# Kernel optimization log

Measured on AMD Instinct MI355X. Metric: run time of the kernel, lower is better.

## Reference

```python
import jax, jax.numpy as jnp
import numpy as np

B, S, H, I, L, NH = 1, 256, 384, 1536, 2, 8

def _gelu(x):
    return jax.nn.gelu(x, approximate=False)  # torch nn.GELU default = exact erf

def _ln(x, g, b, eps=1e-5):
    m = x.mean(-1, keepdims=True)
    v = jnp.var(x, axis=-1, keepdims=True)
    return (x - m) / jnp.sqrt(v + eps) * g + b

def _mha(x, Wqkv, bqkv, Wo, bo):
    b_, s_, h_ = x.shape
    d = h_ // NH
    qkv = x @ Wqkv.T + bqkv  # [B,S,3H]
    q, k, v = jnp.split(qkv, 3, axis=-1)
    sp = lambda t: t.reshape(b_, s_, NH, d).transpose(0, 2, 1, 3)  # [B,NH,S,d]
    q, k, v = sp(q), sp(k), sp(v)
    att = jax.nn.softmax(jnp.einsum('bhqd,bhkd->bhqk', q * (1.0 / np.sqrt(d)), k), axis=-1)
    o = jnp.einsum('bhqk,bhkd->bhqd', att, v).transpose(0, 2, 1, 3).reshape(b_, s_, h_)
    return o @ Wo.T + bo

def _forward(hidden_states, Wqkv, bqkv, Wo, bo, W1, b1, W2, b2, g1, be1, g2, be2,
             Wbil, bbil, Wc1, bc1, Wc2, bc2, Wih, bih, Whh, bhh, Wp1, bp1, Wp2, bp2,
             Wout, bout, reasoning_steps):
    x = hidden_states
    rstate = jnp.zeros((x.shape[0], x.shape[-1]), x.dtype)
    cprobs, conts = [], []
    for _ in range(reasoning_steps):
        # symbolic reasoning layers (eval mode: dropout off)
        for l in range(L):
            x = _ln(x + _mha(x, Wqkv[l], bqkv[l], Wo[l], bo[l]), g1[l], be1[l])
            ff = _gelu(x @ W1[l].T + b1[l]) @ W2[l].T + b2[l]
            x = _ln(x + ff, g2[l], be2[l])
        # contradiction detector: bilinear over all token pairs
        tmp = jnp.einsum('bix,oxy->bioy', x, Wbil)            # [B,S,H,H]
        inter = jnp.einsum('bioy,bjy->bijo', tmp, x) + bbil   # [B,S,S,H]
        h1 = _gelu(inter @ Wc1.T + bc1)                       # [B,S,S,H]
        logits = jnp.einsum('bijh,h->bij', h1, Wc2[0]) + bc2[0]
        cprobs.append(jax.nn.sigmoid(logits))
        # recursive reasoning controller (GRUCell on mean-pooled states)
        pooled = x.mean(axis=1)
        gi = pooled @ Wih.T + bih
        gh = rstate @ Whh.T + bhh
        ir, iz, inn = jnp.split(gi, 3, axis=-1)
        hr, hz, hn = jnp.split(gh, 3, axis=-1)
        r = jax.nn.sigmoid(ir + hr)
        z = jax.nn.sigmoid(iz + hz)
        n = jnp.tanh(inn + r * hn)
        rstate = (1.0 - z) * n + z * rstate
        conts.append(jax.nn.sigmoid(_gelu(rstate @ Wp1.T + bp1) @ Wp2[0] + bp2[0]))
    final = x @ Wout.T + bout
    return final, jnp.stack(cprobs), jnp.stack(conts)

def setup_inputs():
    key = jax.random.key(0)
    ks = iter(jax.random.split(key, 40))
    rn = lambda shape, s=0.02: jax.random.normal(next(ks), shape, jnp.float32) * s
    return {
        'hidden_states': jax.random.normal(next(ks), (B, S, H), jnp.float32),
        'Wqkv': rn((L, 3 * H, H)), 'bqkv': jnp.zeros((L, 3 * H)),
        'Wo': rn((L, H, H)), 'bo': jnp.zeros((L, H)),
        'W1': rn((L, I, H)), 'b1': jnp.zeros((L, I)),
        'W2': rn((L, H, I)), 'b2': jnp.zeros((L, H)),
        'g1': jnp.ones((L, H)), 'be1': jnp.zeros((L, H)),
        'g2': jnp.ones((L, H)), 'be2': jnp.zeros((L, H)),
        'Wbil': rn((H, H, H)), 'bbil': jnp.zeros((H,)),
        'Wc1': rn((H, H)), 'bc1': jnp.zeros((H,)),
        'Wc2': rn((1, H)), 'bc2': jnp.zeros((1,)),
        'Wih': rn((3 * H, H)), 'bih': jnp.zeros((3 * H,)),
        'Whh': rn((3 * H, H)), 'bhh': jnp.zeros((3 * H,)),
        'Wp1': rn((H, H)), 'bp1': jnp.zeros((H,)),
        'Wp2': rn((1, H)), 'bp2': jnp.zeros((1,)),
        'Wout': rn((H, H)), 'bout': jnp.zeros((H,)),
        'reasoning_steps': 2,
    }

def reference(hidden_states, Wqkv, bqkv, Wo, bo, W1, b1, W2, b2, g1, be1, g2, be2,
              Wbil, bbil, Wc1, bc1, Wc2, bc2, Wih, bih, Whh, bhh, Wp1, bp1, Wp2, bp2,
              Wout, bout, reasoning_steps):
    return _forward(hidden_states, Wqkv, bqkv, Wo, bo, W1, b1, W2, b2, g1, be1, g2, be2,
                    Wbil, bbil, Wc1, bc1, Wc2, bc2, Wih, bih, Whh, bhh, Wp1, bp1, Wp2, bp2,
                    Wout, bout, reasoning_steps)
```

## Files before the change

### kernel.cpp

```cpp
#include <hip/hip_runtime.h>

typedef __attribute__((ext_vector_type(4))) float f32x4;
typedef __attribute__((ext_vector_type(8))) short s16x8;

#define DEVI __device__ __forceinline__

DEVI float b2f(short s) {
  union { float f; unsigned u; } v; v.u = ((unsigned)(unsigned short)s) << 16; return v.f;
}
DEVI short f2b(float f) {
  union { float f; unsigned u; } v; v.f = f;
  unsigned u = v.u;
  u += 0x7FFFu + ((u >> 16) & 1u);
  return (short)(u >> 16);
}
DEVI float gelu_f(float x) {
  float z2 = 1.5957691216f * x * (1.0f + 0.044715f * x * x);
  float e = __expf(z2);
  float th = 1.0f - 2.0f / (e + 1.0f);
  return 0.5f * x * (1.0f + th);
}
DEVI float sigm_f(float x) { return 1.0f / (1.0f + expf(-x)); }

DEVI void gld16(const short* g, const short* l) {
  __builtin_amdgcn_global_load_lds((const __attribute__((address_space(1))) void*)g,
                                   (__attribute__((address_space(3))) void*)l, 16, 0, 0);
}

template<bool BIAS, bool OUT_BF16>
__global__ __launch_bounds__(512)
void gemm256_k(const short* __restrict__ A, const short* __restrict__ B,
               const float* __restrict__ bias, void* __restrict__ Cv,
               int N, int K,
               long long sA, long long sB, long long sC)
{
  __shared__ short As[2][256 * 32];
  __shared__ short Bs[2][128 * 32];
  const int bz = blockIdx.z;
  const int n0 = blockIdx.x * 128;
  const int t = threadIdx.x, lane = t & 63, wave = t >> 6;
  const int wm = wave >> 1, wn = wave & 1;
  const short* Ab = A + bz * sA;
  const short* Bb = B + bz * sB;
  const int lr = lane >> 2;
  const int lc = (lane & 3) * 8;
  const int fr = lane & 15, fs = lane >> 4;

  f32x4 acc[4][4];
#pragma unroll
  for (int i = 0; i < 4; ++i)
#pragma unroll
    for (int j = 0; j < 4; ++j) acc[i][j] = f32x4{0.f, 0.f, 0.f, 0.f};

  auto stage = [&](int b, int k0) {
#pragma unroll
    for (int q = 0; q < 2; ++q)
      gld16(Ab + (long long)(q * 128 + wave * 16 + lr) * K + k0 + lc,
            &As[b][(q * 128 + wave * 16) * 32]);
    gld16(Bb + (long long)(n0 + wave * 16 + lr) * K + k0 + lc,
          &Bs[b][wave * 16 * 32]);
  };

  const int NT = K >> 5;
  stage(0, 0);
  __syncthreads();
  for (int tt = 0; tt < NT; ++tt) {
    const int cur = tt & 1;
    if (tt + 1 < NT) stage(cur ^ 1, (tt + 1) << 5);
    s16x8 af[4], bfv[4];
#pragma unroll
    for (int i = 0; i < 4; ++i) af[i]  = *(const s16x8*)&As[cur][(wm * 64 + i * 16 + fr) * 32 + fs * 8];
#pragma unroll
    for (int j = 0; j < 4; ++j) bfv[j] = *(const s16x8*)&Bs[cur][(wn * 64 + j * 16 + fr) * 32 + fs * 8];
#pragma unroll
    for (int i = 0; i < 4; ++i)
#pragma unroll
      for (int j = 0; j < 4; ++j)
        acc[i][j] = __builtin_amdgcn_mfma_f32_16x16x32_bf16(af[i], bfv[j], acc[i][j], 0, 0, 0);
    if (tt + 1 < NT) __syncthreads();
  }

#pragma unroll
  for (int i = 0; i < 4; ++i) {
    int rowb = wm * 64 + i * 16 + fs * 4;
#pragma unroll
    for (int j = 0; j < 4; ++j) {
      int col = n0 + wn * 64 + j * 16 + fr;
      float bb = BIAS ? bias[col] : 0.0f;
#pragma unroll
      for (int u = 0; u < 4; ++u) {
        float v = acc[i][j][u] + bb;
        long long off = bz * sC + (long long)(rowb + u) * N + col;
        if constexpr (OUT_BF16) ((short*)Cv)[off] = f2b(v);
        else                    ((float*)Cv)[off] = v;
      }
    }
  }
}

__global__ __launch_bounds__(512)
void h1log256_k(const short* __restrict__ inter, const short* __restrict__ Wc1b,
                const float* __restrict__ bc1, const float* __restrict__ Wc2,
                const float* __restrict__ bc2, float* __restrict__ outp)
{
  __shared__ short As[2][256 * 32];
  __shared__ short Bs[2][128 * 32];
  __shared__ float part[256][2];
  const int ib = blockIdx.x;
  const int t = threadIdx.x, lane = t & 63, wave = t >> 6;
  const int wm = wave >> 1, wn = wave & 1;
  const short* Ab = inter + (long long)ib * 98304;
  const int lr = lane >> 2;
  const int lc = (lane & 3) * 8;
  const int fr = lane & 15, fs = lane >> 4;

  float lp[16];
#pragma unroll
  for (int e = 0; e < 16; ++e) lp[e] = 0.f;

  for (int n0 = 0; n0 < 384; n0 += 128) {
    f32x4 acc[4][4];
#pragma unroll
    for (int i = 0; i < 4; ++i)
#pragma unroll
      for (int j = 0; j < 4; ++j) acc[i][j] = f32x4{0.f, 0.f, 0.f, 0.f};

    auto stage = [&](int b, int k0) {
#pragma unroll
      for (int q = 0; q < 2; ++q)
        gld16(Ab + (long long)(q * 128 + wave * 16 + lr) * 384 + k0 + lc,
              &As[b][(q * 128 + wave * 16) * 32]);
      gld16(Wc1b + (long long)(n0 + wave * 16 + lr) * 384 + k0 + lc,
            &Bs[b][wave * 16 * 32]);
    };

    stage(0, 0);
    __syncthreads();
    for (int tt = 0; tt < 12; ++tt) {
      const int cur = tt & 1;
      if (tt + 1 < 12) stage(cur ^ 1, (tt + 1) << 5);
      s16x8 af[4], bfv[4];
#pragma unroll
      for (int i = 0; i < 4; ++i) af[i]  = *(const s16x8*)&As[cur][(wm * 64 + i * 16 + fr) * 32 + fs * 8];
#pragma unroll
      for (int j = 0; j < 4; ++j) bfv[j] = *(const s16x8*)&Bs[cur][(wn * 64 + j * 16 + fr) * 32 + fs * 8];
#pragma unroll
      for (int i = 0; i < 4; ++i)
#pragma unroll
        for (int j = 0; j < 4; ++j)
          acc[i][j] = __builtin_amdgcn_mfma_f32_16x16x32_bf16(af[i], bfv[j], acc[i][j], 0, 0, 0);
      if (tt + 1 < 12) __syncthreads();
    }
#pragma unroll
    for (int i = 0; i < 4; ++i)
#pragma unroll
      for (int j = 0; j < 4; ++j) {
        int col = n0 + wn * 64 + j * 16 + fr;
        float w2 = Wc2[col], b1v = bc1[col];
#pragma unroll
        for (int u = 0; u < 4; ++u)
          lp[i * 4 + u] += gelu_f(acc[i][j][u] + b1v) * w2;
      }
    __syncthreads();
  }
#pragma unroll
  for (int m = 1; m < 16; m <<= 1)
#pragma unroll
    for (int e = 0; e < 16; ++e) lp[e] += __shfl_xor(lp[e], m);
  if (fr == 0) {
#pragma unroll
    for (int e = 0; e < 16; ++e)
      part[wm * 64 + (e >> 2) * 16 + fs * 4 + (e & 3)][wn] = lp[e];
  }
  __syncthreads();
  if (t < 256) outp[ib * 256 + t] = sigm_f(part[t][0] + part[t][1] + bc2[0]);
}

template<bool BIAS, bool GELU_ACT, bool OUT_BF16>
__global__ __launch_bounds__(256)
void gemm64_k(const short* __restrict__ A, const short* __restrict__ B,
              const float* __restrict__ bias, void* __restrict__ Cv,
              int M, int N, int K)
{
  __shared__ short As[2][64 * 32];
  __shared__ short Bs[2][64 * 32];
  const int n0 = blockIdx.x * 64;
  const int m0 = blockIdx.y * 64;
  const int t = threadIdx.x, lane = t & 63, wave = t >> 6;
  const int wm = wave >> 1, wn = wave & 1;
  const int srow = lane >> 2;
  const int scol = (lane & 3) * 8;
  const int fr = lane & 15, fs = lane >> 4;

  f32x4 acc[2][2];
#pragma unroll
  for (int i = 0; i < 2; ++i)
#pragma unroll
    for (int j = 0; j < 2; ++j) acc[i][j] = f32x4{0.f, 0.f, 0.f, 0.f};

  auto stage = [&](int b, int k0) {
    gld16(A + (long long)(m0 + wave * 16 + srow) * K + k0 + scol, &As[b][wave * 512]);
    gld16(B + (long long)(n0 + wave * 16 + srow) * K + k0 + scol, &Bs[b][wave * 512]);
  };

  const int NT = K >> 5;
  stage(0, 0);
  __syncthreads();
  for (int tt = 0; tt < NT; ++tt) {
    const int cur = tt & 1;
    if (tt + 1 < NT) stage(cur ^ 1, (tt + 1) << 5);
    s16x8 af[2], bfv[2];
#pragma unroll
    for (int i = 0; i < 2; ++i) af[i]  = *(const s16x8*)&As[cur][(wm * 32 + i * 16 + fr) * 32 + fs * 8];
#pragma unroll
    for (int j = 0; j < 2; ++j) bfv[j] = *(const s16x8*)&Bs[cur][(wn * 32 + j * 16 + fr) * 32 + fs * 8];
#pragma unroll
    for (int i = 0; i < 2; ++i)
#pragma unroll
      for (int j = 0; j < 2; ++j)
        acc[i][j] = __builtin_amdgcn_mfma_f32_16x16x32_bf16(af[i], bfv[j], acc[i][j], 0, 0, 0);
    if (tt + 1 < NT) __syncthreads();
  }

#pragma unroll
  for (int i = 0; i < 2; ++i) {
    int rowb = m0 + wm * 32 + i * 16 + fs * 4;
#pragma unroll
    for (int j = 0; j < 2; ++j) {
      int col = n0 + wn * 32 + j * 16 + fr;
      float bb = BIAS ? bias[col] : 0.0f;
#pragma unroll
      for (int u = 0; u < 4; ++u) {
        float v = acc[i][j][u] + bb;
        if constexpr (GELU_ACT) v = gelu_f(v);
        long long off = (long long)(rowb + u) * N + col;
        if constexpr (OUT_BF16) ((short*)Cv)[off] = f2b(v);
        else                    ((float*)Cv)[off] = v;
      }
    }
  }
}

__global__ __launch_bounds__(256)
void transpose_k(const float* __restrict__ W, short* __restrict__ WT)
{
  __shared__ short L[64 * 68];
  const int o  = blockIdx.z;
  const int x0 = blockIdx.x * 64, y0 = blockIdx.y * 64;
  const float* Wo = W  + (long long)o * 147456;
  short*      WTo = WT + (long long)o * 147456;
  const int t  = threadIdx.x;
  const int rr = t >> 4;
  const int cc = (t & 15) * 4;
#pragma unroll
  for (int q = 0; q < 4; ++q) {
    int xl = rr + 16 * q;
    float4 v = *(const float4*)(Wo + (x0 + xl) * 384 + y0 + cc);
    short4 p; p.x = f2b(v.x); p.y = f2b(v.y); p.z = f2b(v.z); p.w = f2b(v.w);
    *(short4*)&L[xl * 68 + cc] = p;
  }
  __syncthreads();
#pragma unroll
  for (int q = 0; q < 4; ++q) {
    int yl = rr + 16 * q;
    short4 p;
    p.x = L[(cc + 0) * 68 + yl];
    p.y = L[(cc + 1) * 68 + yl];
    p.z = L[(cc + 2) * 68 + yl];
    p.w = L[(cc + 3) * 68 + yl];
    *(short4*)(WTo + (y0 + yl) * 384 + x0 + cc) = p;
  }
}

__global__ __launch_bounds__(256)
void convw_k(const float* __restrict__ W, short* __restrict__ Wb, int n)
{
  int i = (blockIdx.x * 256 + threadIdx.x) * 4;
  if (i < n) {
    float4 v = *(const float4*)(W + i);
    short4 p; p.x = f2b(v.x); p.y = f2b(v.y); p.z = f2b(v.z); p.w = f2b(v.w);
    *(short4*)(Wb + i) = p;
  }
}

__global__ __launch_bounds__(256)
void attn_k(const float* __restrict__ qkv, short* __restrict__ outb)
{
  __shared__ short Ks[256 * 48];
  __shared__ short Vs[256 * 48];
  __shared__ float Ps[32][258];
  const int h  = blockIdx.y;
  const int q0 = blockIdx.x * 32;
  const int t = threadIdx.x, lane = t & 63, wave = t >> 6;
  for (int idx = t; idx < 256 * 48; idx += 256) {
    int j = idx / 48, d = idx - j * 48;
    Ks[idx] = f2b(qkv[j * 1152 + 384 + h * 48 + d]);
    Vs[idx] = f2b(qkv[j * 1152 + 768 + h * 48 + d]);
  }
  __syncthreads();
  const int part = lane & 7;
  const int rl   = wave * 8 + (lane >> 3);
  const int row  = q0 + rl;
  float q[48];
#pragma unroll
  for (int d = 0; d < 48; ++d) q[d] = qkv[row * 1152 + h * 48 + d] * 0.14433756729740644f;
  float mx = -1e30f;
  for (int jj = 0; jj < 32; ++jj) {
    int j = jj * 8 + part;
    float a = 0.f;
#pragma unroll
    for (int dd = 0; dd < 12; ++dd) {
      short4 kk = *(const short4*)&Ks[j * 48 + dd * 4];
      a += q[dd*4+0]*b2f(kk.x) + q[dd*4+1]*b2f(kk.y) + q[dd*4+2]*b2f(kk.z) + q[dd*4+3]*b2f(kk.w);
    }
    Ps[rl][j] = a;
    mx = fmaxf(mx, a);
  }
  mx = fmaxf(mx, __shfl_xor(mx, 1));
  mx = fmaxf(mx, __shfl_xor(mx, 2));
  mx = fmaxf(mx, __shfl_xor(mx, 4));
  float sum = 0.f;
  for (int jj = 0; jj < 32; ++jj) {
    int j = jj * 8 + part;
    float e = expf(Ps[rl][j] - mx);
    Ps[rl][j] = e;
    sum += e;
  }
  sum += __shfl_xor(sum, 1); sum += __shfl_xor(sum, 2); sum += __shfl_xor(sum, 4);
  const float inv = 1.f / sum;
  __syncthreads();
  float o[6] = {0.f, 0.f, 0.f, 0.f, 0.f, 0.f};
  const int vb = part * 6;
  for (int j = 0; j < 256; ++j) {
    float p = Ps[rl][j];
    int base = j * 48 + vb;
#pragma unroll
    for (int dd = 0; dd < 3; ++dd) {
      short2 vv = *(const short2*)&Vs[base + dd * 2];
      o[dd*2]   += p * b2f(vv.x);
      o[dd*2+1] += p * b2f(vv.y);
    }
  }
#pragma unroll
  for (int d = 0; d < 6; ++d) outb[row * 384 + h * 48 + vb + d] = f2b(o[d] * inv);
}

__global__ __launch_bounds__(128)
void ln_k(const float* __restrict__ x, const float* __restrict__ d,
          const float* __restrict__ g, const float* __restrict__ b,
          float* __restrict__ xo, short* __restrict__ xob)
{
  const int row = blockIdx.x, t = threadIdx.x;
  float v[3]; float s = 0.f, ss = 0.f;
#pragma unroll
  for (int i = 0; i < 3; ++i) {
    int c = t + 128 * i;
    float u = x[row * 384 + c] + d[row * 384 + c];
    v[i] = u; s += u; ss += u * u;
  }
#pragma unroll
  for (int m = 1; m < 64; m <<= 1) { s += __shfl_xor(s, m); ss += __shfl_xor(ss, m); }
  __shared__ float sh[4];
  if ((t & 63) == 0) { sh[(t >> 6) * 2] = s; sh[(t >> 6) * 2 + 1] = ss; }
  __syncthreads();
  s = sh[0] + sh[2]; ss = sh[1] + sh[3];
  float mean = s * (1.f / 384.f);
  float var  = ss * (1.f / 384.f) - mean * mean;
  float rstd = rsqrtf(var + 1e-5f);
#pragma unroll
  for (int i = 0; i < 3; ++i) {
    int c = t + 128 * i;
    float y = (v[i] - mean) * rstd * g[c] + b[c];
    xo[row * 384 + c]  = y;
    xob[row * 384 + c] = f2b(y);
  }
}

__global__ void init_k(const float* __restrict__ hs, float* __restrict__ x,
                       short* __restrict__ xb, float* __restrict__ rstate)
{
  int i = blockIdx.x * 256 + threadIdx.x;
  if (i < 98304) { float v = hs[i]; x[i] = v; xb[i] = f2b(v); }
  if (i < 384) rstate[i] = 0.f;
}

__global__ __launch_bounds__(384)
void pool1_k(const float* __restrict__ x, float* __restrict__ partial)
{
  const int t = threadIdx.x, p = blockIdx.x;
  float s = 0.f;
  const float* xr = x + p * 32 * 384;
#pragma unroll 4
  for (int i = 0; i < 32; ++i) s += xr[i * 384 + t];
  partial[p * 384 + t] = s;
}

__global__ __launch_bounds__(256)
void gih_k(const float* __restrict__ Wih, const float* __restrict__ bih,
           const float* __restrict__ Whh, const float* __restrict__ bhh,
           const float* __restrict__ partial, const float* __restrict__ rstate,
           float* __restrict__ gi, float* __restrict__ gh)
{
  const int t = threadIdx.x, lane = t & 63, wave = t >> 6;
  const int r = blockIdx.x * 4 + wave;
  float a = 0.f, b = 0.f;
#pragma unroll
  for (int e = 0; e < 6; ++e) {
    int c = lane + 64 * e;
    float pc = 0.f;
#pragma unroll
    for (int p = 0; p < 8; ++p) pc += partial[p * 384 + c];
    pc *= (1.f / 256.f);
    a += Wih[r * 384 + c] * pc;
    b += Whh[r * 384 + c] * rstate[c];
  }
#pragma unroll
  for (int m = 1; m < 64; m <<= 1) { a += __shfl_xor(a, m); b += __shfl_xor(b, m); }
  if (lane == 0) { gi[r] = a + bih[r]; gh[r] = b + bhh[r]; }
}

__global__ __launch_bounds__(384)
void gru2_k(const float* __restrict__ gi, const float* __restrict__ gh,
            float* __restrict__ rstate, float* __restrict__ hnew)
{
  const int t = threadIdx.x;
  float r = sigm_f(gi[t] + gh[t]);
  float z = sigm_f(gi[384 + t] + gh[384 + t]);
  float n = tanhf(gi[768 + t] + r * gh[768 + t]);
  float h = (1.f - z) * n + z * rstate[t];
  rstate[t] = h;
  hnew[t] = h;
}

__global__ __launch_bounds__(256)
void p1_k(const float* __restrict__ Wp1, const float* __restrict__ bp1,
          const float* __restrict__ hnew, float* __restrict__ p1)
{
  const int t = threadIdx.x, lane = t & 63, wave = t >> 6;
  const int r = blockIdx.x * 4 + wave;
  float a = 0.f;
#pragma unroll
  for (int e = 0; e < 6; ++e) { int c = lane + 64 * e; a += Wp1[r * 384 + c] * hnew[c]; }
#pragma unroll
  for (int m = 1; m < 64; m <<= 1) a += __shfl_xor(a, m);
  if (lane == 0) p1[r] = gelu_f(a + bp1[r]);
}

__global__ __launch_bounds__(64)
void cont_k(const float* __restrict__ p1, const float* __restrict__ Wp2,
            const float* __restrict__ bp2, float* __restrict__ out_cont)
{
  const int lane = threadIdx.x;
  float a = 0.f;
#pragma unroll
  for (int e = 0; e < 6; ++e) { int c = lane + 64 * e; a += p1[c] * Wp2[c]; }
#pragma unroll
  for (int m = 1; m < 64; m <<= 1) a += __shfl_xor(a, m);
  if (lane == 0) out_cont[0] = sigm_f(a + bp2[0]);
}

extern "C" void kernel_launch(void* const* d_in, const int* in_sizes, int n_in,
                              void* d_out, int out_size, void* d_ws, size_t ws_size,
                              hipStream_t stream)
{
  const float* hs   = (const float*)d_in[0];
  const float* Wqkv = (const float*)d_in[1];
  const float* bqkv = (const float*)d_in[2];
  const float* Wo   = (const float*)d_in[3];
  const float* bo   = (const float*)d_in[4];
  const float* W1   = (const float*)d_in[5];
  const float* b1   = (const float*)d_in[6];
  const float* W2   = (const float*)d_in[7];
  const float* b2   = (const float*)d_in[8];
  const float* g1   = (const float*)d_in[9];
  const float* be1  = (const float*)d_in[10];
  const float* g2   = (const float*)d_in[11];
  const float* be2  = (const float*)d_in[12];
  const float* Wbil = (const float*)d_in[13];
  const float* bbil = (const float*)d_in[14];
  const float* Wc1  = (const float*)d_in[15];
  const float* bc1  = (const float*)d_in[16];
  const float* Wc2  = (const float*)d_in[17];
  const float* bc2  = (const float*)d_in[18];
  const float* Wih  = (const float*)d_in[19];
  const float* bih  = (const float*)d_in[20];
  const float* Whh  = (const float*)d_in[21];
  const float* bhh  = (const float*)d_in[22];
  const float* Wp1  = (const float*)d_in[23];
  const float* bp1  = (const float*)d_in[24];
  const float* Wp2  = (const float*)d_in[25];
  const float* bp2  = (const float*)d_in[26];
  const float* Wout = (const float*)d_in[27];
  const float* bout = (const float*)d_in[28];
  float* out = (float*)d_out;

  char* ws = (char*)d_ws;
  size_t off = 0;
  auto alloc = [&](size_t bytes) -> char* {
    char* p = ws + off; off += (bytes + 255) & ~(size_t)255; return p;
  };
  short* wbilT   = (short*)alloc(56623104ULL * 2);
  short* tmp     = (short*)alloc(256ULL * 147456 * 2);
  short* inter   = (short*)alloc(256ULL * 98304 * 2);
  float* x       = (float*)alloc(98304 * 4);
  short* xb      = (short*)alloc(98304 * 2);
  float* qkv     = (float*)alloc(294912 * 4);
  short* attnb   = (short*)alloc(98304 * 2);
  float* delta   = (float*)alloc(98304 * 4);
  short* ff1b    = (short*)alloc(393216 * 2);
  float* rstate  = (float*)alloc(384 * 4);
  float* partial = (float*)alloc(8 * 384 * 4);
  float* gi      = (float*)alloc(1152 * 4);
  float* gh      = (float*)alloc(1152 * 4);
  float* hnew    = (float*)alloc(384 * 4);
  float* p1buf   = (float*)alloc(384 * 4);
  short* wc1b    = (short*)alloc(147456 * 2);
  short* wqkvb   = (short*)alloc(884736ULL * 2);
  short* wob     = (short*)alloc(294912ULL * 2);
  short* w1b     = (short*)alloc(1179648ULL * 2);
  short* w2b     = (short*)alloc(1179648ULL * 2);
  short* woutb   = (short*)alloc(147456 * 2);
  (void)ws_size; (void)in_sizes; (void)n_in; (void)out_size;

  dim3 B256(256);
  dim3 B512(512);

  init_k<<<dim3(384), B256, 0, stream>>>(hs, x, xb, rstate);
  transpose_k<<<dim3(6, 6, 384), B256, 0, stream>>>(Wbil, wbilT);
  convw_k<<<dim3(144),  B256, 0, stream>>>(Wc1, wc1b, 147456);
  convw_k<<<dim3(864),  B256, 0, stream>>>(Wqkv, wqkvb, 884736);
  convw_k<<<dim3(288),  B256, 0, stream>>>(Wo, wob, 294912);
  convw_k<<<dim3(1152), B256, 0, stream>>>(W1, w1b, 1179648);
  convw_k<<<dim3(1152), B256, 0, stream>>>(W2, w2b, 1179648);
  convw_k<<<dim3(144),  B256, 0, stream>>>(Wout, woutb, 147456);

  for (int s = 0; s < 2; ++s) {
    for (int l = 0; l < 2; ++l) {
      gemm64_k<true, false, false><<<dim3(18, 4), B256, 0, stream>>>(
          xb, wqkvb + l * 442368, bqkv + l * 1152, qkv, 256, 1152, 384);
      attn_k<<<dim3(8, 8), B256, 0, stream>>>(qkv, attnb);
      gemm64_k<true, false, false><<<dim3(6, 4), B256, 0, stream>>>(
          attnb, wob + l * 147456, bo + l * 384, delta, 256, 384, 384);
      ln_k<<<dim3(256), dim3(128), 0, stream>>>(x, delta, g1 + l * 384, be1 + l * 384, x, xb);
      gemm64_k<true, true, true><<<dim3(24, 4), B256, 0, stream>>>(
          xb, w1b + l * 589824, b1 + l * 1536, ff1b, 256, 1536, 384);
      gemm64_k<true, false, false><<<dim3(6, 4), B256, 0, stream>>>(
          ff1b, w2b + l * 589824, b2 + l * 384, delta, 256, 384, 1536);
      ln_k<<<dim3(256), dim3(128), 0, stream>>>(x, delta, g2 + l * 384, be2 + l * 384, x, xb);
    }
    gemm256_k<false, true><<<dim3(1152, 1, 1), B512, 0, stream>>>(
        xb, wbilT, (const float*)nullptr, tmp, 147456, 384, 0, 0, 0);
    gemm256_k<true, true><<<dim3(3, 1, 256), B512, 0, stream>>>(
        xb, tmp, bbil, inter, 384, 384, 0, 147456LL, 98304LL);
    h1log256_k<<<dim3(256), B512, 0, stream>>>(inter, wc1b, bc1, Wc2, bc2,
                                               out + 98304 + s * 65536);
    pool1_k<<<dim3(8), dim3(384), 0, stream>>>(x, partial);
    gih_k<<<dim3(288), B256, 0, stream>>>(Wih, bih, Whh, bhh, partial, rstate, gi, gh);
    gru2_k<<<dim3(1), dim3(384), 0, stream>>>(gi, gh, rstate, hnew);
    p1_k<<<dim3(96), B256, 0, stream>>>(Wp1, bp1, hnew, p1buf);
    cont_k<<<dim3(1), dim3(64), 0, stream>>>(p1buf, Wp2, bp2, out + 98304 + 131072 + s);
  }
  gemm64_k<true, false, false><<<dim3(6, 4), B256, 0, stream>>>(
      xb, woutb, bout, out, 256, 384, 384);
}
```

Measured before the change: 671.9 us.

## Fuse output GEMMs with LayerNorm, merge weight conversions and GRU tail kernels

```diff
diff --git a/kernel.cpp b/kernel.cpp
--- a/kernel.cpp
+++ b/kernel.cpp
@@ -176,6 +176,91 @@
   if (t < 256) outp[ib * 256 + t] = sigm_f(part[t][0] + part[t][1] + bc2[0]);
 }
 
+__global__ __launch_bounds__(512)
+void gemmln_k(const short* __restrict__ A, const short* __restrict__ B,
+              const float* __restrict__ bias,
+              const float* __restrict__ xin, float* __restrict__ xout,
+              short* __restrict__ xbout,
+              const float* __restrict__ g, const float* __restrict__ be,
+              int K)
+{
+  __shared__ __align__(16) char ldsbuf[53248];
+  short* As0 = (short*)ldsbuf;
+  short* Bs0 = (short*)(ldsbuf + 4096);
+  float (*u)[385] = (float(*)[385])ldsbuf;
+
+  const int m0 = blockIdx.x * 32;
+  const int t = threadIdx.x, lane = t & 63, wave = t >> 6;
+  const int wm = wave >> 2, wn = wave & 3;
+  const int lr = lane >> 2;
+  const int lc = (lane & 3) * 8;
+  const int fr = lane & 15, fs = lane >> 4;
+
+  f32x4 acc[6];
+#pragma unroll
+  for (int j = 0; j < 6; ++j) acc[j] = f32x4{0.f, 0.f, 0.f, 0.f};
+
+  auto stage = [&](int b, int k0) {
+#pragma unroll
+    for (int q = 0; q < 3; ++q)
+      gld16(B + (long long)(wave * 48 + q * 16 + lr) * K + k0 + lc,
+            &Bs0[b * 12288 + (wave * 48 + q * 16) * 32]);
+    if (wave < 2)
+      gld16(A + (long long)(m0 + wave * 16 + lr) * K + k0 + lc,
+            &As0[b * 1024 + wave * 16 * 32]);
+  };
+
+  const int NT = K >> 5;
+  stage(0, 0);
+  __syncthreads();
+  for (int tt = 0; tt < NT; ++tt) {
+    const int cur = tt & 1;
+    if (tt + 1 < NT) stage(cur ^ 1, (tt + 1) << 5);
+    s16x8 af = *(const s16x8*)&As0[cur * 1024 + (wm * 16 + fr) * 32 + fs * 8];
+    s16x8 bfv[6];
+#pragma unroll
+    for (int j = 0; j < 6; ++j)
+      bfv[j] = *(const s16x8*)&Bs0[cur * 12288 + (wn * 96 + j * 16 + fr) * 32 + fs * 8];
+#pragma unroll
+    for (int j = 0; j < 6; ++j)
+      acc[j] = __builtin_amdgcn_mfma_f32_16x16x32_bf16(af, bfv[j], acc[j], 0, 0, 0);
+    __syncthreads();
+  }
+
+#pragma unroll
+  for (int j = 0; j < 6; ++j) {
+    int col = wn * 96 + j * 16 + fr;
+    float bb = bias[col];
+#pragma unroll
+    for (int q = 0; q < 4; ++q)
+      u[wm * 16 + fs * 4 + q][col] = acc[j][q] + bb;
+  }
+  __syncthreads();
+
+  const int r = t >> 4, c16 = t & 15;
+  const float* xr = xin + (long long)(m0 + r) * 384;
+  float ru[24]; float s = 0.f, ss = 0.f;
+#pragma unroll
+  for (int e = 0; e < 24; ++e) {
+    int col = c16 + 16 * e;
+    float uv = u[r][col] + xr[col];
+    ru[e] = uv; s += uv; ss += uv * uv;
+  }
+#pragma unroll
+  for (int m = 1; m < 16; m <<= 1) { s += __shfl_xor(s, m); ss += __shfl_xor(ss, m); }
+  float mean = s * (1.f / 384.f);
+  float var  = ss * (1.f / 384.f) - mean * mean;
+  float rstd = rsqrtf(var + 1e-5f);
+  float* xo  = xout  + (long long)(m0 + r) * 384;
+  short* xbo = xbout + (long long)(m0 + r) * 384;
+#pragma unroll
+  for (int e = 0; e < 24; ++e) {
+    int col = c16 + 16 * e;
+    float y = (ru[e] - mean) * rstd * g[col] + be[col];
+    xo[col] = y; xbo[col] = f2b(y);
+  }
+}
+
 template<bool BIAS, bool GELU_ACT, bool OUT_BF16>
 __global__ __launch_bounds__(256)
 void gemm64_k(const short* __restrict__ A, const short* __restrict__ B,
@@ -273,14 +358,26 @@
 }
 
 __global__ __launch_bounds__(256)
-void convw_k(const float* __restrict__ W, short* __restrict__ Wb, int n)
-{
-  int i = (blockIdx.x * 256 + threadIdx.x) * 4;
-  if (i < n) {
-    float4 v = *(const float4*)(W + i);
-    short4 p; p.x = f2b(v.x); p.y = f2b(v.y); p.z = f2b(v.z); p.w = f2b(v.w);
-    *(short4*)(Wb + i) = p;
-  }
+void convall_k(const float* __restrict__ Wc1, const float* __restrict__ Wqkv,
+               const float* __restrict__ Wo, const float* __restrict__ W1,
+               const float* __restrict__ W2, const float* __restrict__ Wout,
+               short* __restrict__ Dc1, short* __restrict__ Dqkv,
+               short* __restrict__ Do, short* __restrict__ D1,
+               short* __restrict__ D2, short* __restrict__ Dout)
+{
+  long long i4 = ((long long)blockIdx.x * 256 + threadIdx.x) * 4;
+  const float* s; short* d; long long off;
+  if      (i4 <  147456) { s = Wc1;  d = Dc1;  off = 0; }
+  else if (i4 < 1032192) { s = Wqkv; d = Dqkv; off = 147456; }
+  else if (i4 < 1327104) { s = Wo;   d = Do;   off = 1032192; }
+  else if (i4 < 2506752) { s = W1;   d = D1;   off = 1327104; }
+  else if (i4 < 3686400) { s = W2;   d = D2;   off = 2506752; }
+  else if (i4 < 3833856) { s = Wout; d = Dout; off = 3686400; }
+  else return;
+  long long l = i4 - off;
+  float4 v = *(const float4*)(s + l);
+  short4 p; p.x = f2b(v.x); p.y = f2b(v.y); p.z = f2b(v.z); p.w = f2b(v.w);
+  *(short4*)(d + l) = p;
 }
 
 __global__ __launch_bounds__(256)
@@ -292,10 +389,15 @@
   const int h  = blockIdx.y;
   const int q0 = blockIdx.x * 32;
   const int t = threadIdx.x, lane = t & 63, wave = t >> 6;
-  for (int idx = t; idx < 256 * 48; idx += 256) {
-    int j = idx / 48, d = idx - j * 48;
-    Ks[idx] = f2b(qkv[j * 1152 + 384 + h * 48 + d]);
-    Vs[idx] = f2b(qkv[j * 1152 + 768 + h * 48 + d]);
+  for (int idx = t; idx < 3072; idx += 256) {
+    int j = idx / 12, d4 = (idx - (idx / 12) * 12) * 4;
+    const float* base = qkv + j * 1152 + h * 48 + d4;
+    float4 kv = *(const float4*)(base + 384);
+    float4 vv = *(const float4*)(base + 768);
+    short4 pk; pk.x = f2b(kv.x); pk.y = f2b(kv.y); pk.z = f2b(kv.z); pk.w = f2b(kv.w);
+    short4 pv; pv.x = f2b(vv.x); pv.y = f2b(vv.y); pv.z = f2b(vv.z); pv.w = f2b(vv.w);
+    *(short4*)&Ks[j * 48 + d4] = pk;
+    *(short4*)&Vs[j * 48 + d4] = pv;
   }
   __syncthreads();
   const int part = lane & 7;
@@ -345,37 +447,6 @@
   for (int d = 0; d < 6; ++d) outb[row * 384 + h * 48 + vb + d] = f2b(o[d] * inv);
 }
 
-__global__ __launch_bounds__(128)
-void ln_k(const float* __restrict__ x, const float* __restrict__ d,
-          const float* __restrict__ g, const float* __restrict__ b,
-          float* __restrict__ xo, short* __restrict__ xob)
-{
-  const int row = blockIdx.x, t = threadIdx.x;
-  float v[3]; float s = 0.f, ss = 0.f;
-#pragma unroll
-  for (int i = 0; i < 3; ++i) {
-    int c = t + 128 * i;
-    float u = x[row * 384 + c] + d[row * 384 + c];
-    v[i] = u; s += u; ss += u * u;
-  }
-#pragma unroll
-  for (int m = 1; m < 64; m <<= 1) { s += __shfl_xor(s, m); ss += __shfl_xor(ss, m); }
-  __shared__ float sh[4];
-  if ((t & 63) == 0) { sh[(t >> 6) * 2] = s; sh[(t >> 6) * 2 + 1] = ss; }
-  __syncthreads();
-  s = sh[0] + sh[2]; ss = sh[1] + sh[3];
-  float mean = s * (1.f / 384.f);
-  float var  = ss * (1.f / 384.f) - mean * mean;
-  float rstd = rsqrtf(var + 1e-5f);
-#pragma unroll
-  for (int i = 0; i < 3; ++i) {
-    int c = t + 128 * i;
-    float y = (v[i] - mean) * rstd * g[c] + b[c];
-    xo[row * 384 + c]  = y;
-    xob[row * 384 + c] = f2b(y);
-  }
-}
-
 __global__ void init_k(const float* __restrict__ hs, float* __restrict__ x,
                        short* __restrict__ xb, float* __restrict__ rstate)
 {
@@ -419,44 +490,41 @@
   if (lane == 0) { gi[r] = a + bih[r]; gh[r] = b + bhh[r]; }
 }
 
-__global__ __launch_bounds__(384)
-void gru2_k(const float* __restrict__ gi, const float* __restrict__ gh,
-            float* __restrict__ rstate, float* __restrict__ hnew)
-{
-  const int t = threadIdx.x;
-  float r = sigm_f(gi[t] + gh[t]);
-  float z = sigm_f(gi[384 + t] + gh[384 + t]);
-  float n = tanhf(gi[768 + t] + r * gh[768 + t]);
-  float h = (1.f - z) * n + z * rstate[t];
-  rstate[t] = h;
-  hnew[t] = h;
-}
-
-__global__ __launch_bounds__(256)
-void p1_k(const float* __restrict__ Wp1, const float* __restrict__ bp1,
-          const float* __restrict__ hnew, float* __restrict__ p1)
-{
+__global__ __launch_bounds__(512)
+void gru_tail_k(const float* __restrict__ gi, const float* __restrict__ gh,
+                float* __restrict__ rstate,
+                const float* __restrict__ Wp1, const float* __restrict__ bp1,
+                const float* __restrict__ Wp2, const float* __restrict__ bp2,
+                float* __restrict__ out_cont)
+{
+  __shared__ float hnew[384], p1s[384];
   const int t = threadIdx.x, lane = t & 63, wave = t >> 6;
-  const int r = blockIdx.x * 4 + wave;
-  float a = 0.f;
-#pragma unroll
-  for (int e = 0; e < 6; ++e) { int c = lane + 64 * e; a += Wp1[r * 384 + c] * hnew[c]; }
-#pragma unroll
-  for (int m = 1; m < 64; m <<= 1) a += __shfl_xor(a, m);
-  if (lane == 0) p1[r] = gelu_f(a + bp1[r]);
-}
-
-__global__ __launch_bounds__(64)
-void cont_k(const float* __restrict__ p1, const float* __restrict__ Wp2,
-            const float* __restrict__ bp2, float* __restrict__ out_cont)
-{
-  const int lane = threadIdx.x;
-  float a = 0.f;
-#pragma unroll
-  for (int e = 0; e < 6; ++e) { int c = lane + 64 * e; a += p1[c] * Wp2[c]; }
-#pragma unroll
-  for (int m = 1; m < 64; m <<= 1) a += __shfl_xor(a, m);
-  if (lane == 0) out_cont[0] = sigm_f(a + bp2[0]);
+  if (t < 384) {
+    float r = sigm_f(gi[t] + gh[t]);
+    float z = sigm_f(gi[384 + t] + gh[384 + t]);
+    float n = tanhf(gi[768 + t] + r * gh[768 + t]);
+    float hh = (1.f - z) * n + z * rstate[t];
+    rstate[t] = hh;
+    hnew[t] = hh;
+  }
+  __syncthreads();
+  for (int r = wave; r < 384; r += 8) {
+    float a = 0.f;
+#pragma unroll
+    for (int e = 0; e < 6; ++e) { int c = lane + 64 * e; a += Wp1[r * 384 + c] * hnew[c]; }
+#pragma unroll
+    for (int m = 1; m < 64; m <<= 1) a += __shfl_xor(a, m);
+    if (lane == 0) p1s[r] = gelu_f(a + bp1[r]);
+  }
+  __syncthreads();
+  if (wave == 0) {
+    float a = 0.f;
+#pragma unroll
+    for (int e = 0; e < 6; ++e) { int c = lane + 64 * e; a += p1s[c] * Wp2[c]; }
+#pragma unroll
+    for (int m = 1; m < 64; m <<= 1) a += __shfl_xor(a, m);
+    if (lane == 0) out_cont[0] = sigm_f(a + bp2[0]);
+  }
 }
 
 extern "C" void kernel_launch(void* const* d_in, const int* in_sizes, int n_in,
@@ -506,14 +574,11 @@
   short* xb      = (short*)alloc(98304 * 2);
   float* qkv     = (float*)alloc(294912 * 4);
   short* attnb   = (short*)alloc(98304 * 2);
-  float* delta   = (float*)alloc(98304 * 4);
   short* ff1b    = (short*)alloc(393216 * 2);
   float* rstate  = (float*)alloc(384 * 4);
   float* partial = (float*)alloc(8 * 384 * 4);
   float* gi      = (float*)alloc(1152 * 4);
   float* gh      = (float*)alloc(1152 * 4);
-  float* hnew    = (float*)alloc(384 * 4);
-  float* p1buf   = (float*)alloc(384 * 4);
   short* wc1b    = (short*)alloc(147456 * 2);
   short* wqkvb   = (short*)alloc(884736ULL * 2);
   short* wob     = (short*)alloc(294912ULL * 2);
@@ -527,26 +592,22 @@
 
   init_k<<<dim3(384), B256, 0, stream>>>(hs, x, xb, rstate);
   transpose_k<<<dim3(6, 6, 384), B256, 0, stream>>>(Wbil, wbilT);
-  convw_k<<<dim3(144),  B256, 0, stream>>>(Wc1, wc1b, 147456);
-  convw_k<<<dim3(864),  B256, 0, stream>>>(Wqkv, wqkvb, 884736);
-  convw_k<<<dim3(288),  B256, 0, stream>>>(Wo, wob, 294912);
-  convw_k<<<dim3(1152), B256, 0, stream>>>(W1, w1b, 1179648);
-  convw_k<<<dim3(1152), B256, 0, stream>>>(W2, w2b, 1179648);
-  convw_k<<<dim3(144),  B256, 0, stream>>>(Wout, woutb, 147456);
+  convall_k<<<dim3(3744), B256, 0, stream>>>(Wc1, Wqkv, Wo, W1, W2, Wout,
+                                             wc1b, wqkvb, wob, w1b, w2b, woutb);
 
   for (int s = 0; s < 2; ++s) {
     for (int l = 0; l < 2; ++l) {
       gemm64_k<true, false, false><<<dim3(18, 4), B256, 0, stream>>>(
           xb, wqkvb + l * 442368, bqkv + l * 1152, qkv, 256, 1152, 384);
       attn_k<<<dim3(8, 8), B256, 0, stream>>>(qkv, attnb);
-      gemm64_k<true, false, false><<<dim3(6, 4), B256, 0, stream>>>(
-          attnb, wob + l * 147456, bo + l * 384, delta, 256, 384, 384);
-      ln_k<<<dim3(256), dim3(128), 0, stream>>>(x, delta, g1 + l * 384, be1 + l * 384, x, xb);
+      gemmln_k<<<dim3(8), B512, 0, stream>>>(
+          attnb, wob + l * 147456, bo + l * 384, x, x, xb,
+          g1 + l * 384, be1 + l * 384, 384);
       gemm64_k<true, true, true><<<dim3(24, 4), B256, 0, stream>>>(
           xb, w1b + l * 589824, b1 + l * 1536, ff1b, 256, 1536, 384);
-      gemm64_k<true, false, false><<<dim3(6, 4), B256, 0, stream>>>(
-          ff1b, w2b + l * 589824, b2 + l * 384, delta, 256, 384, 1536);
-      ln_k<<<dim3(256), dim3(128), 0, stream>>>(x, delta, g2 + l * 384, be2 + l * 384, x, xb);
+      gemmln_k<<<dim3(8), B512, 0, stream>>>(
+          ff1b, w2b + l * 589824, b2 + l * 384, x, x, xb,
+          g2 + l * 384, be2 + l * 384, 1536);
     }
     gemm256_k<false, true><<<dim3(1152, 1, 1), B512, 0, stream>>>(
         xb, wbilT, (const float*)nullptr, tmp, 147456, 384, 0, 0, 0);
@@ -556,9 +617,8 @@
                                                out + 98304 + s * 65536);
     pool1_k<<<dim3(8), dim3(384), 0, stream>>>(x, partial);
     gih_k<<<dim3(288), B256, 0, stream>>>(Wih, bih, Whh, bhh, partial, rstate, gi, gh);
-    gru2_k<<<dim3(1), dim3(384), 0, stream>>>(gi, gh, rstate, hnew);
-    p1_k<<<dim3(96), B256, 0, stream>>>(Wp1, bp1, hnew, p1buf);
-    cont_k<<<dim3(1), dim3(64), 0, stream>>>(p1buf, Wp2, bp2, out + 98304 + 131072 + s);
+    gru_tail_k<<<dim3(1), B512, 0, stream>>>(gi, gh, rstate, Wp1, bp1, Wp2, bp2,
+                                             out + 98304 + 131072 + s);
   }
   gemm64_k<true, false, false><<<dim3(6, 4), B256, 0, stream>>>(
       xb, woutb, bout, out, 256, 384, 384);
```

Result: slower. 806.8 us (+20.1%).
